# Performance work log

Measured on AMD Instinct MI355X. Metric: run time of the kernel, lower is better.

Reference implementation:

```python
import jax, jax.numpy as jnp
import numpy as np

D_MODEL = 512
N_HEAD = 8
D_HEAD = D_MODEL // N_HEAD


def _linear(x, W, b):
    return x @ W + b


def setup_inputs() -> dict:
    key = jax.random.key(0)
    ks = jax.random.split(key, 20)
    B, N, D = 8, 1024, D_MODEL
    H = D // 2
    s = 1.0 / np.sqrt(D)
    s2 = 1.0 / np.sqrt(H)
    inp = {
        'query': jax.random.normal(ks[0], (B, N, D), jnp.float32),
        'key_in': jax.random.normal(ks[1], (B, N, D), jnp.float32),
        'value': jax.random.normal(ks[2], (B, N, D), jnp.float32),
        'Wq': jax.random.normal(ks[3], (D, D), jnp.float32) * s,
        'bq': jnp.zeros((D,), jnp.float32),
        'Wk': jax.random.normal(ks[4], (D, D), jnp.float32) * s,
        'bk': jnp.zeros((D,), jnp.float32),
        'Wv': jax.random.normal(ks[5], (D, D), jnp.float32) * s,
        'bv': jnp.zeros((D,), jnp.float32),
        'Wo': jax.random.normal(ks[6], (D, D), jnp.float32) * s,
        'bo': jnp.zeros((D,), jnp.float32),
        'Ws1': jax.random.normal(ks[7], (D, H), jnp.float32) * s,
        'bs1': jnp.zeros((H,), jnp.float32),
        'Ws2': jax.random.normal(ks[8], (H, D), jnp.float32) * s2,
        'bs2': jnp.zeros((D,), jnp.float32),
        'Wc1': jax.random.normal(ks[9], (D, H), jnp.float32) * s,
        'bc1': jnp.zeros((H,), jnp.float32),
        'Wc2': jax.random.normal(ks[10], (H, D), jnp.float32) * s2,
        'bc2': jnp.zeros((D,), jnp.float32),
    }
    return inp


def reference(query, key_in, value, Wq, bq, Wk, bk, Wv, bv, Wo, bo,
              Ws1, bs1, Ws2, bs2, Wc1, bc1, Wc2, bc2):
    B, N, D = query.shape
    H, Dh = N_HEAD, D_HEAD

    def split_heads(x):  # [b, n, h*d] -> [b, h, n, d]
        return x.reshape(B, N, H, Dh).transpose(0, 2, 1, 3)

    q = split_heads(_linear(query, Wq, bq))
    k = split_heads(_linear(key_in, Wk, bk))
    vv = _linear(value, Wv, bv)  # [b, n, d] == rearrange(v,'b h n d->b n (h d)')

    # spatial gating: Linear-ReLU-Linear-Sigmoid on w_v(value)
    sw = jax.nn.sigmoid(_linear(jax.nn.relu(_linear(vv, Ws1, bs1)), Ws2, bs2))
    v_spatial = split_heads(vv * sw)

    # channel gating: MLP on mean-over-seq profile, broadcast back to seq
    prof = value.mean(axis=1, keepdims=True)  # [b, 1, d]
    cw = jax.nn.sigmoid(_linear(jax.nn.relu(_linear(prof, Wc1, bc1)), Wc2, bc2))
    v_channel = split_heads(_linear(value * cw, Wv, bv))

    v_dual = v_spatial + v_channel

    scores = jnp.einsum('bhqd,bhkd->bhqk', q, k) / np.sqrt(Dh).astype(np.float32)
    attn = jax.nn.softmax(scores, axis=-1)
    out = jnp.einsum('bhqk,bhkd->bhqd', attn, v_dual)
    out = out.transpose(0, 2, 1, 3).reshape(B, N, D)
    return _linear(out, Wo, bo)  # dropout is identity in eval mode
```

## Files before the change

### kernel.cpp

```cpp
#include <hip/hip_runtime.h>

typedef unsigned short u16t;
typedef __bf16  bf8   __attribute__((ext_vector_type(8)));
typedef float   f32x4 __attribute__((ext_vector_type(4)));
typedef unsigned short us4 __attribute__((ext_vector_type(4)));

#define DEV __device__ __forceinline__

DEV float bf2f(u16t u) { union { unsigned u; float f; } x; x.u = ((unsigned)u) << 16; return x.f; }
DEV u16t  f2bf(float f) {
    union { float f; unsigned u; } x; x.f = f;
    unsigned r = x.u + 0x7FFFu + ((x.u >> 16) & 1u);
    return (u16t)(r >> 16);
}
DEV uint4 pack8(const float* v) {
    uint4 r;
    r.x = (unsigned)f2bf(v[0]) | ((unsigned)f2bf(v[1]) << 16);
    r.y = (unsigned)f2bf(v[2]) | ((unsigned)f2bf(v[3]) << 16);
    r.z = (unsigned)f2bf(v[4]) | ((unsigned)f2bf(v[5]) << 16);
    r.w = (unsigned)f2bf(v[6]) | ((unsigned)f2bf(v[7]) << 16);
    return r;
}
DEV void gll16(const void* g, void* l) {
    __builtin_amdgcn_global_load_lds(
        (const __attribute__((address_space(1))) unsigned*)g,
        (__attribute__((address_space(3))) unsigned*)l, 16, 0, 0);
}

#define DMODEL 512
#define SEQ    1024
#define NBATCH 8

__global__ __launch_bounds__(256) void fill_sentinel(float* out, int n)
{
    int i = blockIdx.x * 256 + threadIdx.x;
    if (i < n) out[i] = 100.f;
}

__global__ __launch_bounds__(256) void cvt3(const float* q, const float* k,
                                            const float* v,
                                            u16t* Qb, u16t* Kb, u16t* Vb)
{
    int y = blockIdx.y;
    const float* s = (y == 0) ? q : (y == 1) ? k : v;
    u16t*        d = (y == 0) ? Qb : (y == 1) ? Kb : Vb;
    size_t i = ((size_t)blockIdx.x * 256 + threadIdx.x) * 8;
    float4 a = *(const float4*)(s + i), b = *(const float4*)(s + i + 4);
    float o[8] = {a.x, a.y, a.z, a.w, b.x, b.y, b.z, b.w};
    *(uint4*)&d[i] = pack8(o);
}

__global__ __launch_bounds__(256) void transpose6(
    const float* s0, const float* s1, const float* s2, const float* s3,
    const float* s4, const float* s5,
    u16t* d0, u16t* d1, u16t* d2, u16t* d3, u16t* d4, u16t* d5)
{
    int z = blockIdx.z;
    const float* S; u16t* D; int R, C;
    switch (z) {
        case 0: S = s0; D = d0; R = 512; C = 512; break;
        case 1: S = s1; D = d1; R = 512; C = 512; break;
        case 2: S = s2; D = d2; R = 512; C = 512; break;
        case 3: S = s3; D = d3; R = 512; C = 512; break;
        case 4: S = s4; D = d4; R = 512; C = 256; break;
        default:S = s5; D = d5; R = 256; C = 512; break;
    }
    int c0 = blockIdx.x * 32, r0 = blockIdx.y * 32;
    if (c0 >= C || r0 >= R) return;
    __shared__ u16t tile[32][33];
    int tx = threadIdx.x & 31, ty = threadIdx.x >> 5;
#pragma unroll
    for (int p = 0; p < 4; ++p) {
        int r = ty + p * 8;
        tile[r][tx] = f2bf(S[(size_t)(r0 + r) * C + c0 + tx]);
    }
    __syncthreads();
#pragma unroll
    for (int p = 0; p < 4; ++p) {
        int r = ty + p * 8;
        D[(size_t)(c0 + r) * R + r0 + tx] = tile[tx][r];
    }
}

__global__ __launch_bounds__(256) void colmean(const u16t* Vi, float* prof)
{
    int b = blockIdx.y, z = blockIdx.z;
    int d = blockIdx.x * 256 + threadIdx.x;
    const u16t* p = Vi + (size_t)b * SEQ * DMODEL + (size_t)z * 64 * DMODEL + d;
    float s = 0.f;
#pragma unroll 8
    for (int n = 0; n < 64; ++n) s += bf2f(p[(size_t)n * DMODEL]);
    atomicAdd(&prof[b * DMODEL + d], s * (1.f / 1024.f));
}

__global__ __launch_bounds__(256) void cmlp(const float* prof,
                                            const float* Wc1, const float* bc1,
                                            const float* Wc2, const float* bc2,
                                            u16t* cw)
{
    int b = blockIdx.x, t = threadIdx.x;
    __shared__ float pf[512];
    __shared__ float hf[256];
    pf[t]       = prof[b * 512 + t];
    pf[t + 256] = prof[b * 512 + t + 256];
    __syncthreads();
    float s = bc1[t];
    for (int k = 0; k < 512; ++k) s += pf[k] * Wc1[(size_t)k * 256 + t];
    hf[t] = fmaxf(s, 0.f);
    __syncthreads();
#pragma unroll
    for (int o = 0; o < 2; ++o) {
        int d = t + o * 256;
        float s2 = bc2[d];
        for (int k = 0; k < 256; ++k) s2 += hf[k] * Wc2[(size_t)k * 512 + d];
        cw[b * 512 + d] = f2bf(1.f / (1.f + __expf(-s2)));
    }
}

__global__ __launch_bounds__(256) void scale_wv(const u16t* WvT, const u16t* cw,
                                                u16t* WvTs)
{
    int b = blockIdx.y;
    int idx = blockIdx.x * 2048 + threadIdx.x * 8;
    int k = idx & 511;
    uint4 wv = *(const uint4*)&WvT[idx];
    uint4 cu = *(const uint4*)&cw[b * 512 + k];
    const u16t* wp = (const u16t*)&wv;
    const u16t* cp = (const u16t*)&cu;
    float o[8];
#pragma unroll
    for (int q = 0; q < 8; ++q) o[q] = bf2f(wp[q]) * bf2f(cp[q]);
    *(uint4*)&WvTs[(size_t)b * 262144 + idx] = pack8(o);
}

template<int MINW, int WR, int WC, int WM, int NT>
__global__ __launch_bounds__(256, MINW) void gemmP(
    const u16t* A0, const u16t* A1, const u16t* A2, const u16t* A3,
    const u16t* W0, const u16t* W1, const u16t* W2, const u16t* W3,
    const float* B0, const float* B1, const float* B2, const float* B3,
    void* C0, void* C1, void* C2, void* C3,
    int N, int K, int mode,
    const u16t* VVp, u16t* VdTp,
    int tmask, int outf32, int wbmask)
{
    constexpr int BM = WR * WM * 16;
    constexpr int BN = WC * NT * 16;
    constexpr int PA = BM / 64;
    constexpr int PB = BN / 64;
    constexpr int LPT = PA + PB;

    int z = blockIdx.z;
    const u16t* A  = (z == 0) ? A0 : (z == 1) ? A1 : (z == 2) ? A2 : A3;
    const u16t* W  = (z == 0) ? W0 : (z == 1) ? W1 : (z == 2) ? W2 : W3;
    const float* Bi = (z == 0) ? B0 : (z == 1) ? B1 : (z == 2) ? B2 : B3;
    void*       C  = (z == 0) ? C0 : (z == 1) ? C1 : (z == 2) ? C2 : C3;

    int tstore = (tmask >> z) & 1;

    int tid = threadIdx.x;
    int w = tid >> 6, lane = tid & 63, quad = lane >> 4, l16 = lane & 15;
    int wr = w / WC, wc = w % WC;
    int m0 = blockIdx.x * BM, n0 = blockIdx.y * BN;
    int bb = m0 >> 10;
    if ((wbmask >> z) & 1) W += (size_t)bb * 262144;

    __shared__ __align__(16) u16t As[3][BM * 32];
    __shared__ __align__(16) u16t Bs[3][BN * 32];

    const u16t* srcA[PA];
#pragma unroll
    for (int p = 0; p < PA; ++p) {
        int ci = p * 256 + tid, r = ci >> 2, g = ci & 3;
        srcA[p] = A + (size_t)(m0 + r) * K + (g ^ (r & 3)) * 8;
    }
    const u16t* srcB[PB];
#pragma unroll
    for (int p = 0; p < PB; ++p) {
        int ci = p * 256 + tid, r = ci >> 2, g = ci & 3;
        srcB[p] = W + (size_t)(n0 + r) * K + (g ^ (r & 3)) * 8;
    }

    f32x4 zero = {0.f, 0.f, 0.f, 0.f};
    f32x4 acc[WM][NT];
#pragma unroll
    for (int mi = 0; mi < WM; ++mi)
#pragma unroll
        for (int ni = 0; ni < NT; ++ni) acc[mi][ni] = zero;

    auto stage = [&](int buf, int k0) {
#pragma unroll
        for (int p = 0; p < PA; ++p)
            gll16(srcA[p] + k0, &As[buf][(size_t)(p * 256 + w * 64) * 8]);
#pragma unroll
        for (int p = 0; p < PB; ++p)
            gll16(srcB[p] + k0, &Bs[buf][(size_t)(p * 256 + w * 64) * 8]);
    };
    auto compute = [&](int buf) {
        int sx = l16 & 3;
        bf8 af[WM], bfr[NT];
#pragma unroll
        for (int mi = 0; mi < WM; ++mi)
            af[mi] = *(const bf8*)&As[buf][(wr * WM * 16 + mi * 16 + l16) * 32 + ((quad ^ sx) * 8)];
#pragma unroll
        for (int ni = 0; ni < NT; ++ni)
            bfr[ni] = *(const bf8*)&Bs[buf][(wc * NT * 16 + ni * 16 + l16) * 32 + ((quad ^ sx) * 8)];
#pragma unroll
        for (int mi = 0; mi < WM; ++mi)
#pragma unroll
            for (int ni = 0; ni < NT; ++ni)
                acc[mi][ni] = __builtin_amdgcn_mfma_f32_16x16x32_bf16(af[mi], bfr[ni], acc[mi][ni], 0, 0, 0);
    };

    int nt = K >> 5;
    stage(0, 0);
    stage(1, 32);
    for (int t = 0; t < nt; ++t) {
        if (t + 1 < nt)
            asm volatile("s_waitcnt vmcnt(%0) lgkmcnt(0)" :: "n"(LPT) : "memory");
        else
            asm volatile("s_waitcnt vmcnt(0) lgkmcnt(0)" ::: "memory");
        __builtin_amdgcn_s_barrier();
        __builtin_amdgcn_sched_barrier(0);
        compute(t % 3);
        if (t + 2 < nt) stage((t + 2) % 3, (t + 2) << 5);
    }

#pragma unroll
    for (int mi = 0; mi < WM; ++mi) {
        int grow0 = m0 + wr * WM * 16 + mi * 16 + quad * 4;
#pragma unroll
        for (int ni = 0; ni < NT; ++ni) {
            int gcol = n0 + wc * NT * 16 + ni * 16 + l16;
            float bias = Bi[gcol];
            if (mode == 2) {
                int h = gcol >> 6, dh = gcol & 63;
                int b_ = grow0 >> 10, n_ = grow0 & 1023;
                size_t tbase = (size_t)((b_ * 8 + h) * 64 + dh) * 1024 + n_;
                us4 vc = *(const us4*)&VdTp[tbase];
                us4 pk;
#pragma unroll
                for (int r = 0; r < 4; ++r) {
                    float s = acc[mi][ni][r] + bias;
                    float sw = 1.f / (1.f + __expf(-s));
                    float vvv = bf2f(VVp[(size_t)(grow0 + r) * DMODEL + gcol]);
                    pk[r] = f2bf(vvv * sw + bf2f(vc[r]));
                }
                *(us4*)&VdTp[tbase] = pk;
            } else if (tstore) {
                int h = gcol >> 6, dh = gcol & 63;
                int b_ = grow0 >> 10, n_ = grow0 & 1023;
                us4 pk;
#pragma unroll
                for (int r = 0; r < 4; ++r) pk[r] = f2bf(acc[mi][ni][r] + bias);
                *(us4*)&((u16t*)C)[(size_t)((b_ * 8 + h) * 64 + dh) * 1024 + n_] = pk;
            } else if (outf32) {
#pragma unroll
                for (int r = 0; r < 4; ++r)
                    ((float*)C)[(size_t)(grow0 + r) * N + gcol] = acc[mi][ni][r] + bias;
            } else {
#pragma unroll
                for (int r = 0; r < 4; ++r) {
                    float v = acc[mi][ni][r] + bias;
                    if (mode == 1) v = fmaxf(v, 0.f);
                    ((u16t*)C)[(size_t)(grow0 + r) * N + gcol] = f2bf(v);
                }
            }
        }
    }
}

__global__ __launch_bounds__(256, 2) void attn(const u16t* Q, const u16t* Km,
                                               const u16t* VdT, u16t* Oa)
{
    __shared__ __align__(16) u16t Qs[128 * 64];
    __shared__ __align__(16) u16t Ks[2][128 * 64];
    __shared__ __align__(16) u16t Vs[2][64 * 128];

    int bh = blockIdx.x, qt = blockIdx.y;
    int b = bh >> 3, h = bh & 7;
    int tid = threadIdx.x;
    int w = tid >> 6, lane = tid & 63, quad = lane >> 4, l16 = lane & 15;
    int l7 = l16 & 7;
    int ht = quad >> 1;
    int sA = ((quad & 1) * 32 + l16) * 4;
    int sB = sA + 64;

    const u16t* Qp = Q   + ((size_t)(b * SEQ + qt * 128)) * DMODEL + h * 64;
    const u16t* Kp = Km  + ((size_t)(b * SEQ)) * DMODEL + h * 64;
    const u16t* Vp = VdT + ((size_t)(b * 8 + h)) * 64 * SEQ;

    auto stageKV = [&](int buf, int it) {
#pragma unroll
        for (int p = 0; p < 4; ++p) {
            int ci = p * 256 + tid;
            int rk = ci >> 3, gk = ci & 7;
            gll16(&Kp[(size_t)(it * 128 + rk) * DMODEL + ((gk ^ (rk & 7)) * 8)],
                  &Ks[buf][(size_t)(p * 256 + w * 64) * 8]);
            int rv = ci >> 4, gv = ci & 15;
            gll16(&Vp[(size_t)rv * SEQ + it * 128 + ((gv ^ (rv & 15)) * 8)],
                  &Vs[buf][(size_t)(p * 256 + w * 64) * 8]);
        }
    };

#pragma unroll
    for (int p = 0; p < 4; ++p) {
        int ci = p * 256 + tid;
        int r = ci >> 3, g = ci & 7;
        int gs = (g ^ (r & 7)) * 8;
        gll16(&Qp[(size_t)r * DMODEL + gs], &Qs[(size_t)(p * 256 + w * 64) * 8]);
    }
    stageKV(0, 0);

    asm volatile("s_waitcnt vmcnt(8)" ::: "memory");
    __builtin_amdgcn_s_barrier();
    bf8 aq[2][2];
#pragma unroll
    for (int qg = 0; qg < 2; ++qg)
#pragma unroll
        for (int ks = 0; ks < 2; ++ks)
            aq[qg][ks] = *(const bf8*)&Qs[(w * 32 + qg * 16 + l16) * 64 + (((ks * 4 + quad) ^ l7) * 8)];

    f32x4 zero = {0.f, 0.f, 0.f, 0.f};
    f32x4 oacc[2][4];
    float l_run[2] = {0.f, 0.f};
#pragma unroll
    for (int qg = 0; qg < 2; ++qg)
#pragma unroll
        for (int r = 0; r < 4; ++r) oacc[qg][r] = zero;

    for (int it = 0; it < 8; ++it) {
        int buf = it & 1;
        asm volatile("s_waitcnt vmcnt(0) lgkmcnt(0)" ::: "memory");
        __builtin_amdgcn_s_barrier();
        __builtin_amdgcn_sched_barrier(0);

        if (it + 1 < 8) stageKV(buf ^ 1, it + 1);

#pragma unroll
        for (int kh = 0; kh < 2; ++kh) {
            bf8 bk[2][4];
#pragma unroll
            for (int ks = 0; ks < 2; ++ks) {
                int sG = ((ks * 4 + quad) ^ l7) * 8;
#pragma unroll
                for (int j = 0; j < 4; ++j)
                    bk[ks][j] = *(const bf8*)&Ks[buf][(kh * 64 + j * 16 + l16) * 64 + sG];
            }
            f32x4 sacc[2][4];
#pragma unroll
            for (int qg = 0; qg < 2; ++qg)
#pragma unroll
                for (int j = 0; j < 4; ++j) sacc[qg][j] = zero;
#pragma unroll
            for (int qg = 0; qg < 2; ++qg)
#pragma unroll
                for (int ks = 0; ks < 2; ++ks)
#pragma unroll
                    for (int j = 0; j < 4; ++j)
                        sacc[qg][j] = __builtin_amdgcn_mfma_f32_16x16x32_bf16(bk[ks][j], aq[qg][ks], sacc[qg][j], 0, 0, 0);

            unsigned pks[2][8];
#pragma unroll
            for (int qg = 0; qg < 2; ++qg) {
                float p[4][4];
                float rsum = 0.f;
#pragma unroll
                for (int j = 0; j < 4; ++j)
#pragma unroll
                    for (int r = 0; r < 4; ++r) {
                        float xx = fmaf(sacc[qg][j][r], 0.18033688f, -5.77078016f);
                        float pe;
                        asm("v_exp_f32 %0, %1" : "=v"(pe) : "v"(xx));
                        p[j][r] = pe;
                        rsum += pe;
                    }
                rsum += __shfl_xor(rsum, 16);
                rsum += __shfl_xor(rsum, 32);
                l_run[qg] += rsum;
#pragma unroll
                for (int j = 0; j < 4; ++j)
#pragma unroll
                    for (int c = 0; c < 2; ++c) {
                        union { __bf16 hh[2]; unsigned u; } pk;
                        pk.hh[0] = (__bf16)p[j][2 * c];
                        pk.hh[1] = (__bf16)p[j][2 * c + 1];
                        pks[qg][2 * j + c] = pk.u;
                    }
            }

            bf8 bvf[2][4];
#pragma unroll
            for (int ks = 0; ks < 2; ++ks) {
#pragma unroll
                for (int j = 0; j < 4; ++j) {
                    int rv = j * 16 + l16;
                    int sG = (((kh * 8 + ks * 4 + quad) ^ (rv & 15)) * 8);
                    bvf[ks][j] = *(const bf8*)&Vs[buf][rv * 128 + sG];
                }
            }
#pragma unroll
            for (int qg = 0; qg < 2; ++qg)
#pragma unroll
                for (int ks = 0; ks < 2; ++ks) {
                    int rA[4], rB[4];
#pragma unroll
                    for (int c = 0; c < 4; ++c) {
                        rA[c] = __builtin_amdgcn_ds_bpermute(sA, (int)pks[qg][ks * 4 + c]);
                        rB[c] = __builtin_amdgcn_ds_bpermute(sB, (int)pks[qg][ks * 4 + c]);
                    }
                    union { int d[4]; bf8 v; } apu;
                    apu.d[0] = ht ? rA[2] : rA[0];
                    apu.d[1] = ht ? rA[3] : rA[1];
                    apu.d[2] = ht ? rB[2] : rB[0];
                    apu.d[3] = ht ? rB[3] : rB[1];
#pragma unroll
                    for (int j = 0; j < 4; ++j)
                        oacc[qg][j] = __builtin_amdgcn_mfma_f32_16x16x32_bf16(apu.v, bvf[ks][j], oacc[qg][j], 0, 0, 0);
                }
        }
    }

#pragma unroll
    for (int qg = 0; qg < 2; ++qg) {
        float lr[4];
#pragma unroll
        for (int r4 = 0; r4 < 4; ++r4)
            lr[r4] = __shfl(l_run[qg], (quad << 4) | (quad * 4 + r4));
#pragma unroll
        for (int j = 0; j < 4; ++j) {
#pragma unroll
            for (int r4 = 0; r4 < 4; ++r4) {
                int rq = qt * 128 + w * 32 + qg * 16 + quad * 4 + r4;
                float v = oacc[qg][j][r4] / lr[r4];
                Oa[((size_t)(b * SEQ + rq)) * DMODEL + h * 64 + j * 16 + l16] = f2bf(v);
            }
        }
    }
}

extern "C" void kernel_launch(void* const* d_in, const int* in_sizes, int n_in,
                              void* d_out, int out_size, void* d_ws, size_t ws_size,
                              hipStream_t stream)
{
    const float* query  = (const float*)d_in[0];
    const float* key_in = (const float*)d_in[1];
    const float* value  = (const float*)d_in[2];
    const float* Wq  = (const float*)d_in[3];  const float* bq  = (const float*)d_in[4];
    const float* Wk  = (const float*)d_in[5];  const float* bk  = (const float*)d_in[6];
    const float* Wv  = (const float*)d_in[7];  const float* bv  = (const float*)d_in[8];
    const float* Wo  = (const float*)d_in[9];  const float* bo  = (const float*)d_in[10];
    const float* Ws1 = (const float*)d_in[11]; const float* bs1 = (const float*)d_in[12];
    const float* Ws2 = (const float*)d_in[13]; const float* bs2 = (const float*)d_in[14];
    const float* Wc1 = (const float*)d_in[15]; const float* bc1 = (const float*)d_in[16];
    const float* Wc2 = (const float*)d_in[17]; const float* bc2 = (const float*)d_in[18];
    float* out = (float*)d_out;

    u16t* ws = (u16t*)d_ws;
    u16t* WqT  = ws + 0;
    u16t* WkT  = ws + 262144;
    u16t* WvT  = ws + 524288;
    u16t* WoT  = ws + 786432;
    u16t* Ws1T = ws + 1048576;
    u16t* Ws2T = ws + 1179648;
    u16t* WvTs = ws + 1310720;
    u16t* Vi   = ws + 3407872;
    u16t* Qm   = ws + 7602176;
    u16t* Kmm  = ws + 11796480;
    u16t* VV   = ws + 15990784;
    u16t* VdT  = ws + 20185088;
    u16t* cw   = ws + 24379392;
    float* prof = (float*)(ws + 24383488);
    u16t* Qbf  = ws + 24391680;
    u16t* Kbf  = ws + 28585984;
    u16t* H1 = Vi;
    u16t* Oa = VV;

    const size_t NEED_BYTES = 32780288ull * 2ull;
    if (ws_size < NEED_BYTES) {
        fill_sentinel<<<(out_size + 255) / 256, 256, 0, stream>>>(out, out_size);
        return;
    }

    hipMemsetAsync((void*)prof, 0, NBATCH * DMODEL * sizeof(float), stream);

    cvt3<<<dim3(2048, 3), 256, 0, stream>>>(query, key_in, value, Qbf, Kbf, Vi);
    transpose6<<<dim3(16, 16, 6), 256, 0, stream>>>(Wq, Wk, Wv, Wo, Ws1, Ws2,
                                                    WqT, WkT, WvT, WoT, Ws1T, Ws2T);
    colmean<<<dim3(2, 8, 16), 256, 0, stream>>>(Vi, prof);
    cmlp<<<8, 256, 0, stream>>>(prof, Wc1, bc1, Wc2, bc2, cw);
    scale_wv<<<dim3(128, 8), 256, 0, stream>>>(WvT, cw, WvTs);

    gemmP<2, 2, 2, 4, 8><<<dim3(64, 2, 4), 256, 0, stream>>>(
        Qbf, Kbf, Vi, Vi,
        WqT, WkT, WvT, WvTs,
        bq, bk, bv, bv,
        Qm, Kmm, VV, VdT,
        512, 512, 0, nullptr, VdT,
        0x8, 0, 0x8);

    gemmP<4, 2, 2, 2, 2><<<dim3(128, 4, 1), 256, 0, stream>>>(
        VV, VV, VV, VV, Ws1T, Ws1T, Ws1T, Ws1T, bs1, bs1, bs1, bs1,
        H1, H1, H1, H1, 256, 512, 1, nullptr, nullptr, 0, 0, 0);

    gemmP<4, 2, 2, 2, 2><<<dim3(128, 8, 1), 256, 0, stream>>>(
        H1, H1, H1, H1, Ws2T, Ws2T, Ws2T, Ws2T, bs2, bs2, bs2, bs2,
        Qm, Qm, Qm, Qm,
        512, 256, 2, VV, VdT, 0, 0, 0);

    attn<<<dim3(64, 8), 256, 0, stream>>>(Qm, Kmm, VdT, Oa);

    gemmP<4, 2, 2, 2, 2><<<dim3(128, 8, 1), 256, 0, stream>>>(
        Oa, Oa, Oa, Oa, WoT, WoT, WoT, WoT, bo, bo, bo, bo,
        out, out, out, out, 512, 512, 0, nullptr, nullptr,
        0, 1, 0);
}
```

Measured before the change: 259.8 us.

## Fuse fp32-to-bf16 input conversion into QKV GEMM A-tile loading

Removes the separate cvt3 pass that wrote bf16 copies of query, key and value. The first projection GEMM now loads fp32 A tiles into registers, converts them to bf16 and writes them to LDS, using a two-stage register double buffer alongside the async B loads. colmean now reads fp32 value directly. This saves a full read-write pass over three 16MB inputs, but doubles A-tile global traffic inside the GEMM, raises register pressure and replaces async global-to-LDS loads for A with synchronous ones.

```diff
diff --git a/kernel.cpp b/kernel.cpp
--- a/kernel.cpp
+++ b/kernel.cpp
@@ -35,19 +35,6 @@
 {
     int i = blockIdx.x * 256 + threadIdx.x;
     if (i < n) out[i] = 100.f;
-}
-
-__global__ __launch_bounds__(256) void cvt3(const float* q, const float* k,
-                                            const float* v,
-                                            u16t* Qb, u16t* Kb, u16t* Vb)
-{
-    int y = blockIdx.y;
-    const float* s = (y == 0) ? q : (y == 1) ? k : v;
-    u16t*        d = (y == 0) ? Qb : (y == 1) ? Kb : Vb;
-    size_t i = ((size_t)blockIdx.x * 256 + threadIdx.x) * 8;
-    float4 a = *(const float4*)(s + i), b = *(const float4*)(s + i + 4);
-    float o[8] = {a.x, a.y, a.z, a.w, b.x, b.y, b.z, b.w};
-    *(uint4*)&d[i] = pack8(o);
 }
 
 __global__ __launch_bounds__(256) void transpose6(
@@ -82,14 +69,14 @@
     }
 }
 
-__global__ __launch_bounds__(256) void colmean(const u16t* Vi, float* prof)
+__global__ __launch_bounds__(256) void colmean(const float* V, float* prof)
 {
     int b = blockIdx.y, z = blockIdx.z;
     int d = blockIdx.x * 256 + threadIdx.x;
-    const u16t* p = Vi + (size_t)b * SEQ * DMODEL + (size_t)z * 64 * DMODEL + d;
+    const float* p = V + (size_t)b * SEQ * DMODEL + (size_t)z * 64 * DMODEL + d;
     float s = 0.f;
 #pragma unroll 8
-    for (int n = 0; n < 64; ++n) s += bf2f(p[(size_t)n * DMODEL]);
+    for (int n = 0; n < 64; ++n) s += p[(size_t)n * DMODEL];
     atomicAdd(&prof[b * DMODEL + d], s * (1.f / 1024.f));
 }
 
@@ -133,9 +120,9 @@
     *(uint4*)&WvTs[(size_t)b * 262144 + idx] = pack8(o);
 }
 
-template<int MINW, int WR, int WC, int WM, int NT>
+template<int MINW, int WR, int WC, int WM, int NT, int AF32>
 __global__ __launch_bounds__(256, MINW) void gemmP(
-    const u16t* A0, const u16t* A1, const u16t* A2, const u16t* A3,
+    const void* A0, const void* A1, const void* A2, const void* A3,
     const u16t* W0, const u16t* W1, const u16t* W2, const u16t* W3,
     const float* B0, const float* B1, const float* B2, const float* B3,
     void* C0, void* C1, void* C2, void* C3,
@@ -147,10 +134,10 @@
     constexpr int BN = WC * NT * 16;
     constexpr int PA = BM / 64;
     constexpr int PB = BN / 64;
-    constexpr int LPT = PA + PB;
+    constexpr int WAITN = AF32 ? (2 * PA + PB) : (PA + PB);
 
     int z = blockIdx.z;
-    const u16t* A  = (z == 0) ? A0 : (z == 1) ? A1 : (z == 2) ? A2 : A3;
+    const void* A  = (z == 0) ? A0 : (z == 1) ? A1 : (z == 2) ? A2 : A3;
     const u16t* W  = (z == 0) ? W0 : (z == 1) ? W1 : (z == 2) ? W2 : W3;
     const float* Bi = (z == 0) ? B0 : (z == 1) ? B1 : (z == 2) ? B2 : B3;
     void*       C  = (z == 0) ? C0 : (z == 1) ? C1 : (z == 2) ? C2 : C3;
@@ -167,11 +154,13 @@
     __shared__ __align__(16) u16t As[3][BM * 32];
     __shared__ __align__(16) u16t Bs[3][BN * 32];
 
-    const u16t* srcA[PA];
+    const u16t* srcA16[PA]; const float* srcAf[PA];
 #pragma unroll
     for (int p = 0; p < PA; ++p) {
         int ci = p * 256 + tid, r = ci >> 2, g = ci & 3;
-        srcA[p] = A + (size_t)(m0 + r) * K + (g ^ (r & 3)) * 8;
+        int gs = (g ^ (r & 3)) * 8;
+        srcA16[p] = (const u16t*)A + (size_t)(m0 + r) * K + gs;
+        srcAf[p]  = (const float*)A + (size_t)(m0 + r) * K + gs;
     }
     const u16t* srcB[PB];
 #pragma unroll
@@ -187,13 +176,48 @@
 #pragma unroll
         for (int ni = 0; ni < NT; ++ni) acc[mi][ni] = zero;
 
-    auto stage = [&](int buf, int k0) {
-#pragma unroll
-        for (int p = 0; p < PA; ++p)
-            gll16(srcA[p] + k0, &As[buf][(size_t)(p * 256 + w * 64) * 8]);
+    float4 fa0[PA], fb0[PA], fa1[PA], fb1[PA];
+
+    auto ldA0 = [&](int k0) {
+#pragma unroll
+        for (int p = 0; p < PA; ++p) {
+            fa0[p] = *(const float4*)(srcAf[p] + k0);
+            fb0[p] = *(const float4*)(srcAf[p] + k0 + 4);
+        }
+    };
+    auto ldA1 = [&](int k0) {
+#pragma unroll
+        for (int p = 0; p < PA; ++p) {
+            fa1[p] = *(const float4*)(srcAf[p] + k0);
+            fb1[p] = *(const float4*)(srcAf[p] + k0 + 4);
+        }
+    };
+    auto wrA0 = [&](int buf) {
+#pragma unroll
+        for (int p = 0; p < PA; ++p) {
+            float v[8] = {fa0[p].x, fa0[p].y, fa0[p].z, fa0[p].w,
+                          fb0[p].x, fb0[p].y, fb0[p].z, fb0[p].w};
+            *(uint4*)&As[buf][(size_t)(p * 256 + tid) * 8] = pack8(v);
+        }
+    };
+    auto wrA1 = [&](int buf) {
+#pragma unroll
+        for (int p = 0; p < PA; ++p) {
+            float v[8] = {fa1[p].x, fa1[p].y, fa1[p].z, fa1[p].w,
+                          fb1[p].x, fb1[p].y, fb1[p].z, fb1[p].w};
+            *(uint4*)&As[buf][(size_t)(p * 256 + tid) * 8] = pack8(v);
+        }
+    };
+    auto stageB = [&](int buf, int k0) {
 #pragma unroll
         for (int p = 0; p < PB; ++p)
             gll16(srcB[p] + k0, &Bs[buf][(size_t)(p * 256 + w * 64) * 8]);
+    };
+    auto stageAll = [&](int buf, int k0) {
+#pragma unroll
+        for (int p = 0; p < PA; ++p)
+            gll16(srcA16[p] + k0, &As[buf][(size_t)(p * 256 + w * 64) * 8]);
+        stageB(buf, k0);
     };
     auto compute = [&](int buf) {
         int sx = l16 & 3;
@@ -212,17 +236,41 @@
     };
 
     int nt = K >> 5;
-    stage(0, 0);
-    stage(1, 32);
-    for (int t = 0; t < nt; ++t) {
-        if (t + 1 < nt)
-            asm volatile("s_waitcnt vmcnt(%0) lgkmcnt(0)" :: "n"(LPT) : "memory");
-        else
-            asm volatile("s_waitcnt vmcnt(0) lgkmcnt(0)" ::: "memory");
-        __builtin_amdgcn_s_barrier();
-        __builtin_amdgcn_sched_barrier(0);
-        compute(t % 3);
-        if (t + 2 < nt) stage((t + 2) % 3, (t + 2) << 5);
+    if constexpr (AF32) {
+        ldA0(0); stageB(0, 0);
+        wrA0(0);
+        ldA1(32); stageB(1, 32);
+        for (int t = 0; t < nt; t += 2) {
+            asm volatile("s_waitcnt vmcnt(%0) lgkmcnt(0)" :: "n"(WAITN) : "memory");
+            __builtin_amdgcn_s_barrier();
+            __builtin_amdgcn_sched_barrier(0);
+            compute(t % 3);
+            wrA1((t + 1) % 3);
+            if (t + 2 < nt) { ldA0((t + 2) << 5); stageB((t + 2) % 3, (t + 2) << 5); }
+            int u = t + 1;
+            if (u + 1 < nt)
+                asm volatile("s_waitcnt vmcnt(%0) lgkmcnt(0)" :: "n"(WAITN) : "memory");
+            else
+                asm volatile("s_waitcnt vmcnt(0) lgkmcnt(0)" ::: "memory");
+            __builtin_amdgcn_s_barrier();
+            __builtin_amdgcn_sched_barrier(0);
+            compute(u % 3);
+            if (u + 1 < nt) wrA0((u + 1) % 3);
+            if (u + 2 < nt) { ldA1((u + 2) << 5); stageB((u + 2) % 3, (u + 2) << 5); }
+        }
+    } else {
+        stageAll(0, 0);
+        stageAll(1, 32);
+        for (int t = 0; t < nt; ++t) {
+            if (t + 1 < nt)
+                asm volatile("s_waitcnt vmcnt(%0) lgkmcnt(0)" :: "n"(WAITN) : "memory");
+            else
+                asm volatile("s_waitcnt vmcnt(0) lgkmcnt(0)" ::: "memory");
+            __builtin_amdgcn_s_barrier();
+            __builtin_amdgcn_sched_barrier(0);
+            compute(t % 3);
+            if (t + 2 < nt) stageAll((t + 2) % 3, (t + 2) << 5);
+        }
     }
 
 #pragma unroll
@@ -463,19 +511,16 @@
     u16t* Ws1T = ws + 1048576;
     u16t* Ws2T = ws + 1179648;
     u16t* WvTs = ws + 1310720;
-    u16t* Vi   = ws + 3407872;
+    u16t* H1   = ws + 3407872;
     u16t* Qm   = ws + 7602176;
     u16t* Kmm  = ws + 11796480;
     u16t* VV   = ws + 15990784;
     u16t* VdT  = ws + 20185088;
     u16t* cw   = ws + 24379392;
     float* prof = (float*)(ws + 24383488);
-    u16t* Qbf  = ws + 24391680;
-    u16t* Kbf  = ws + 28585984;
-    u16t* H1 = Vi;
     u16t* Oa = VV;
 
-    const size_t NEED_BYTES = 32780288ull * 2ull;
+    const size_t NEED_BYTES = 24391680ull * 2ull;
     if (ws_size < NEED_BYTES) {
         fill_sentinel<<<(out_size + 255) / 256, 256, 0, stream>>>(out, out_size);
         return;
@@ -483,33 +528,32 @@
 
     hipMemsetAsync((void*)prof, 0, NBATCH * DMODEL * sizeof(float), stream);
 
-    cvt3<<<dim3(2048, 3), 256, 0, stream>>>(query, key_in, value, Qbf, Kbf, Vi);
+    colmean<<<dim3(2, 8, 16), 256, 0, stream>>>(value, prof);
     transpose6<<<dim3(16, 16, 6), 256, 0, stream>>>(Wq, Wk, Wv, Wo, Ws1, Ws2,
                                                     WqT, WkT, WvT, WoT, Ws1T, Ws2T);
-    colmean<<<dim3(2, 8, 16), 256, 0, stream>>>(Vi, prof);
     cmlp<<<8, 256, 0, stream>>>(prof, Wc1, bc1, Wc2, bc2, cw);
     scale_wv<<<dim3(128, 8), 256, 0, stream>>>(WvT, cw, WvTs);
 
-    gemmP<2, 2, 2, 4, 8><<<dim3(64, 2, 4), 256, 0, stream>>>(
-        Qbf, Kbf, Vi, Vi,
+    gemmP<2, 2, 2, 4, 8, 1><<<dim3(64, 2, 4), 256, 0, stream>>>(
+        query, key_in, value, value,
         WqT, WkT, WvT, WvTs,
         bq, bk, bv, bv,
         Qm, Kmm, VV, VdT,
         512, 512, 0, nullptr, VdT,
         0x8, 0, 0x8);
 
-    gemmP<4, 2, 2, 2, 2><<<dim3(128, 4, 1), 256, 0, stream>>>(
+    gemmP<4, 2, 2, 2, 2, 0><<<dim3(128, 4, 1), 256, 0, stream>>>(
         VV, VV, VV, VV, Ws1T, Ws1T, Ws1T, Ws1T, bs1, bs1, bs1, bs1,
         H1, H1, H1, H1, 256, 512, 1, nullptr, nullptr, 0, 0, 0);
 
-    gemmP<4, 2, 2, 2, 2><<<dim3(128, 8, 1), 256, 0, stream>>>(
+    gemmP<4, 2, 2, 2, 2, 0><<<dim3(128, 8, 1), 256, 0, stream>>>(
         H1, H1, H1, H1, Ws2T, Ws2T, Ws2T, Ws2T, bs2, bs2, bs2, bs2,
         Qm, Qm, Qm, Qm,
         512, 256, 2, VV, VdT, 0, 0, 0);
 
     attn<<<dim3(64, 8), 256, 0, stream>>>(Qm, Kmm, VdT, Oa);
 
-    gemmP<4, 2, 2, 2, 2><<<dim3(128, 8, 1), 256, 0, stream>>>(
+    gemmP<4, 2, 2, 2, 2, 0><<<dim3(128, 8, 1), 256, 0, stream>>>(
         Oa, Oa, Oa, Oa, WoT, WoT, WoT, WoT, bo, bo, bo, bo,
         out, out, out, out, 512, 512, 0, nullptr, nullptr,
         0, 1, 0);
```

Result: no change. 261.5 us (+0.7%).

## Fuse input conversion, weight transposes and column mean into one prep kernel

Applied to the files above, without the earlier changes.

Merges the bf16 conversion of q/k/v, the six weight transposes and the column-mean profile into a single launch, with blockIdx.y==3 blocks doing transposes and column sums. The column mean now reads the fp32 value input directly instead of the converted bf16 copy, which removes its dependency on the conversion. The projection GEMM template parameters and grid are also changed (different tiling, more blocks in y). Many blocks in the y==3 row do nothing, and reading fp32 doubles colmean traffic.

```diff
diff --git a/kernel.cpp b/kernel.cpp
--- a/kernel.cpp
+++ b/kernel.cpp
@@ -37,60 +37,62 @@
     if (i < n) out[i] = 100.f;
 }
 
-__global__ __launch_bounds__(256) void cvt3(const float* q, const float* k,
-                                            const float* v,
-                                            u16t* Qb, u16t* Kb, u16t* Vb)
-{
-    int y = blockIdx.y;
-    const float* s = (y == 0) ? q : (y == 1) ? k : v;
-    u16t*        d = (y == 0) ? Qb : (y == 1) ? Kb : Vb;
-    size_t i = ((size_t)blockIdx.x * 256 + threadIdx.x) * 8;
-    float4 a = *(const float4*)(s + i), b = *(const float4*)(s + i + 4);
-    float o[8] = {a.x, a.y, a.z, a.w, b.x, b.y, b.z, b.w};
-    *(uint4*)&d[i] = pack8(o);
-}
-
-__global__ __launch_bounds__(256) void transpose6(
+__global__ __launch_bounds__(256) void prep(
+    const float* q, const float* k, const float* v,
+    u16t* Qb, u16t* Kb, u16t* Vb,
     const float* s0, const float* s1, const float* s2, const float* s3,
     const float* s4, const float* s5,
-    u16t* d0, u16t* d1, u16t* d2, u16t* d3, u16t* d4, u16t* d5)
-{
-    int z = blockIdx.z;
-    const float* S; u16t* D; int R, C;
-    switch (z) {
-        case 0: S = s0; D = d0; R = 512; C = 512; break;
-        case 1: S = s1; D = d1; R = 512; C = 512; break;
-        case 2: S = s2; D = d2; R = 512; C = 512; break;
-        case 3: S = s3; D = d3; R = 512; C = 512; break;
-        case 4: S = s4; D = d4; R = 512; C = 256; break;
-        default:S = s5; D = d5; R = 256; C = 512; break;
-    }
-    int c0 = blockIdx.x * 32, r0 = blockIdx.y * 32;
-    if (c0 >= C || r0 >= R) return;
+    u16t* d0, u16t* d1, u16t* d2, u16t* d3, u16t* d4, u16t* d5,
+    float* prof)
+{
     __shared__ u16t tile[32][33];
-    int tx = threadIdx.x & 31, ty = threadIdx.x >> 5;
-#pragma unroll
-    for (int p = 0; p < 4; ++p) {
-        int r = ty + p * 8;
-        tile[r][tx] = f2bf(S[(size_t)(r0 + r) * C + c0 + tx]);
-    }
-    __syncthreads();
-#pragma unroll
-    for (int p = 0; p < 4; ++p) {
-        int r = ty + p * 8;
-        D[(size_t)(c0 + r) * R + r0 + tx] = tile[tx][r];
-    }
-}
-
-__global__ __launch_bounds__(256) void colmean(const u16t* Vi, float* prof)
-{
-    int b = blockIdx.y, z = blockIdx.z;
-    int d = blockIdx.x * 256 + threadIdx.x;
-    const u16t* p = Vi + (size_t)b * SEQ * DMODEL + (size_t)z * 64 * DMODEL + d;
-    float s = 0.f;
+    int y = blockIdx.y, tid = threadIdx.x;
+    if (y < 3) {
+        const float* s = (y == 0) ? q : (y == 1) ? k : v;
+        u16t*        d = (y == 0) ? Qb : (y == 1) ? Kb : Vb;
+        size_t i = ((size_t)blockIdx.x * 256 + tid) * 8;
+        float4 a = *(const float4*)(s + i), b = *(const float4*)(s + i + 4);
+        float o[8] = {a.x, a.y, a.z, a.w, b.x, b.y, b.z, b.w};
+        *(uint4*)&d[i] = pack8(o);
+        return;
+    }
+    int x = blockIdx.x;
+    if (x < 1536) {
+        int z = x >> 8, rem = x & 255;
+        int bx = rem & 15, by = rem >> 4;
+        const float* S; u16t* D; int R, C;
+        switch (z) {
+            case 0: S = s0; D = d0; R = 512; C = 512; break;
+            case 1: S = s1; D = d1; R = 512; C = 512; break;
+            case 2: S = s2; D = d2; R = 512; C = 512; break;
+            case 3: S = s3; D = d3; R = 512; C = 512; break;
+            case 4: S = s4; D = d4; R = 512; C = 256; break;
+            default:S = s5; D = d5; R = 256; C = 512; break;
+        }
+        int c0 = bx * 32, r0 = by * 32;
+        if (c0 >= C || r0 >= R) return;
+        int tx = tid & 31, ty = tid >> 5;
+#pragma unroll
+        for (int p = 0; p < 4; ++p) {
+            int r = ty + p * 8;
+            tile[r][tx] = f2bf(S[(size_t)(r0 + r) * C + c0 + tx]);
+        }
+        __syncthreads();
+#pragma unroll
+        for (int p = 0; p < 4; ++p) {
+            int r = ty + p * 8;
+            D[(size_t)(c0 + r) * R + r0 + tx] = tile[tx][r];
+        }
+    } else if (x < 1792) {
+        int t = x - 1536;
+        int xb = t & 1, b = (t >> 1) & 7, zb = t >> 4;
+        int d = xb * 256 + tid;
+        const float* p = v + (size_t)b * SEQ * DMODEL + (size_t)zb * 64 * DMODEL + d;
+        float s = 0.f;
 #pragma unroll 8
-    for (int n = 0; n < 64; ++n) s += bf2f(p[(size_t)n * DMODEL]);
-    atomicAdd(&prof[b * DMODEL + d], s * (1.f / 1024.f));
+        for (int n = 0; n < 64; ++n) s += p[(size_t)n * DMODEL];
+        atomicAdd(&prof[b * DMODEL + d], s * (1.f / 1024.f));
+    }
 }
 
 __global__ __launch_bounds__(256) void cmlp(const float* prof,
@@ -483,14 +485,15 @@
 
     hipMemsetAsync((void*)prof, 0, NBATCH * DMODEL * sizeof(float), stream);
 
-    cvt3<<<dim3(2048, 3), 256, 0, stream>>>(query, key_in, value, Qbf, Kbf, Vi);
-    transpose6<<<dim3(16, 16, 6), 256, 0, stream>>>(Wq, Wk, Wv, Wo, Ws1, Ws2,
-                                                    WqT, WkT, WvT, WoT, Ws1T, Ws2T);
-    colmean<<<dim3(2, 8, 16), 256, 0, stream>>>(Vi, prof);
+    prep<<<dim3(2048, 4), 256, 0, stream>>>(
+        query, key_in, value, Qbf, Kbf, Vi,
+        Wq, Wk, Wv, Wo, Ws1, Ws2,
+        WqT, WkT, WvT, WoT, Ws1T, Ws2T,
+        prof);
     cmlp<<<8, 256, 0, stream>>>(prof, Wc1, bc1, Wc2, bc2, cw);
     scale_wv<<<dim3(128, 8), 256, 0, stream>>>(WvT, cw, WvTs);
 
-    gemmP<2, 2, 2, 4, 8><<<dim3(64, 2, 4), 256, 0, stream>>>(
+    gemmP<3, 2, 2, 4, 4><<<dim3(64, 4, 4), 256, 0, stream>>>(
         Qbf, Kbf, Vi, Vi,
         WqT, WkT, WvT, WvTs,
         bq, bk, bv, bv,
```

New measurement: 261.2 us. Within noise of the previous version (+0.5%).
